# Kernel tuning notes

Measured on AMD Instinct MI355X. Metric: run time of the kernel, lower is better.

Reference implementation:

```python
import jax, jax.numpy as jnp
import numpy as np

S, M, H, E = 8192, 1024, 4096, 8
CAPACITY = S // E  # capacity_factor = 1.0, k = 1


def setup_inputs() -> dict:
    key = jax.random.key(0)
    ks = jax.random.split(key, 4)
    return {
        "x": jax.random.normal(ks[0], (S, M), jnp.float32),
        "wg": jax.random.normal(ks[1], (M, E), jnp.float32) * 0.02,
        "inter_w": jax.random.normal(ks[2], (E, M, H), jnp.float32) * 0.02,
        "inter_b": jnp.zeros((E, H), jnp.float32),
        "output_w": jax.random.normal(ks[3], (E, H, M), jnp.float32) * 0.02,
        "output_b": jnp.zeros((E, M), jnp.float32),
    }


def _top1_gate(x, wg, capacity):
    """GShard-style top-1 gate (inference: no noise, drop tokens over capacity).
    Returns combine_weights [S,E,C] (float) and dispatch_mask [S,E,C] (float 0/1)."""
    logits = x @ wg                                   # [S,E]
    gates = jax.nn.softmax(logits, axis=-1)           # [S,E]
    idx = jnp.argmax(gates, axis=-1)                  # [S]
    mask1 = jax.nn.one_hot(idx, gates.shape[-1], dtype=gates.dtype)  # [S,E]
    # 0-based position of each token within its expert's queue
    locations = jnp.cumsum(mask1, axis=0) - mask1     # [S,E]
    mask1 = mask1 * (locations < capacity)            # drop overflow tokens
    pos = jnp.sum(locations * mask1, axis=1).astype(jnp.int32)  # [S]
    gate_s = jnp.sum(gates * mask1, axis=1)           # [S] gate value of kept tokens
    loc_oh = jax.nn.one_hot(pos, capacity, dtype=gates.dtype)    # [S,C]
    combine = gate_s[:, None, None] * mask1[:, :, None] * loc_oh[:, None, :]  # [S,E,C]
    dispatch = (combine > 0).astype(x.dtype)
    return combine, dispatch


def reference(x, wg, inter_w, inter_b, output_w, output_b):
    combine, dispatch = _top1_gate(x, wg, CAPACITY)
    # token dispatch: torch.einsum('sec,sm->ecm', dispatch_mask, attention_output)
    disp_x = jnp.einsum('sec,sm->ecm', dispatch, x)                 # [E,C,M]
    # per-expert fused gelu-GEMM MLP (gelu_gemm_func: gelu(x@W1+b1)@W2, +b2)
    h = jax.nn.gelu(jnp.einsum('ecm,emh->ech', disp_x, inter_w)
                    + inter_b[:, None, :], approximate=False)       # [E,C,H]
    exp_out = jnp.einsum('ech,ehm->ecm', h, output_w) + output_b[:, None, :]  # [E,C,M]
    # combine: combined_weights.reshape(S, E*C) @ expert_output.reshape(E*C, M)
    y = jnp.einsum('sec,ecm->sm', combine, exp_out)                 # [S,M]
    return y
```

## Files before the change

### kernel.cpp

```cpp
#include <hip/hip_runtime.h>

#define S_ 8192
#define M_ 1024
#define H_ 4096
#define E_ 8
#define C_ 1024

typedef short s16x8 __attribute__((ext_vector_type(8)));
typedef float f32x4 __attribute__((ext_vector_type(4)));

__device__ __forceinline__ unsigned short f2bf(float f) {
    unsigned int u = __float_as_uint(f);
    unsigned int r = u + 0x7fffu + ((u >> 16) & 1u);
    return (unsigned short)(r >> 16);
}
__device__ __forceinline__ float bf2f(unsigned short s) {
    return __uint_as_float(((unsigned int)s) << 16);
}

__device__ __forceinline__ void async_copy16(const unsigned short* g, unsigned short* l) {
    __builtin_amdgcn_global_load_lds(
        (const __attribute__((address_space(1))) unsigned int*)g,
        (__attribute__((address_space(3))) unsigned int*)l, 16, 0, 0);
}

__global__ __launch_bounds__(256) void gate_kernel(
    const float* __restrict__ x, const float* __restrict__ wg,
    int* __restrict__ expert_of, float* __restrict__ gate_full,
    unsigned short* __restrict__ xb)
{
    int token = (blockIdx.x * 256 + threadIdx.x) >> 6;
    int lane  = threadIdx.x & 63;
    const float* xr = x + (size_t)token * M_;
    unsigned short* xbr = xb + (size_t)token * M_;
    double acc[E_] = {0,0,0,0,0,0,0,0};
    for (int t = 0; t < M_ / 64; ++t) {
        int m = t * 64 + lane;
        float xf = xr[m];
        xbr[m] = f2bf(xf);
        double xv = (double)xf;
        const float* w = wg + m * E_;
        #pragma unroll
        for (int e = 0; e < E_; ++e) acc[e] += xv * (double)w[e];
    }
    #pragma unroll
    for (int e = 0; e < E_; ++e)
        for (int off = 32; off; off >>= 1) acc[e] += __shfl_xor(acc[e], off);
    if (lane == 0) {
        double mx = acc[0]; int idx = 0;
        #pragma unroll
        for (int e = 1; e < E_; ++e) if (acc[e] > mx) { mx = acc[e]; idx = e; }
        double den = 0.0;
        #pragma unroll
        for (int e = 0; e < E_; ++e) den += exp(acc[e] - mx);
        expert_of[token] = idx;
        gate_full[token] = (float)(1.0 / den);
    }
}

__global__ __launch_bounds__(256) void count_kernel(
    const int* __restrict__ expert_of, int* __restrict__ cnt,
    int* __restrict__ slot_to_token)
{
    __shared__ int wc[4][E_];
    int tid = threadIdx.x, lane = tid & 63, wv = tid >> 6;
    slot_to_token[blockIdx.x * 256 + tid] = -1;
    int e = expert_of[blockIdx.x * 256 + tid];
    #pragma unroll
    for (int j = 0; j < E_; ++j) {
        unsigned long long b = __ballot(e == j);
        if (lane == 0) wc[wv][j] = __popcll(b);
    }
    __syncthreads();
    if (tid < E_) {
        int s = 0;
        #pragma unroll
        for (int w = 0; w < 4; ++w) s += wc[w][tid];
        cnt[blockIdx.x * E_ + tid] = s;
    }
}

__global__ __launch_bounds__(64) void prefix_kernel(
    const int* __restrict__ cnt, int* __restrict__ cbase)
{
    int tid = threadIdx.x;
    if (tid < E_) {
        int run = 0;
        for (int b = 0; b < 32; ++b) { cbase[b * E_ + tid] = run; run += cnt[b * E_ + tid]; }
    }
}

__global__ __launch_bounds__(256) void scatter_kernel(
    const int* __restrict__ expert_of, const int* __restrict__ cbase,
    int* __restrict__ slot_to_token)
{
    __shared__ int wc[4][E_];
    int tid = threadIdx.x, lane = tid & 63, wv = tid >> 6;
    int s = blockIdx.x * 256 + tid;
    int e = expert_of[s];
    unsigned long long mymask = 0;
    #pragma unroll
    for (int j = 0; j < E_; ++j) {
        unsigned long long b = __ballot(e == j);
        if (lane == 0) wc[wv][j] = __popcll(b);
        if (j == e) mymask = b;
    }
    __syncthreads();
    int waveoff = 0;
    for (int w = 0; w < 4; ++w) if (w < wv) waveoff += wc[w][e];
    int pos = cbase[blockIdx.x * E_ + e] + waveoff +
              __popcll(mymask & ((1ull << lane) - 1ull));
    if (pos < C_) slot_to_token[e * C_ + pos] = s;
}

__global__ __launch_bounds__(256) void transpose_cvt_kernel(
    const float* __restrict__ src, unsigned short* __restrict__ dst, int K, int N)
{
    __shared__ unsigned short tile[64 * 84];
    const size_t esz = (size_t)K * N;
    const float* s = src + (size_t)blockIdx.z * esz;
    unsigned short* d = dst + (size_t)blockIdx.z * esz;
    const int k0 = blockIdx.y * 64, n0 = blockIdx.x * 64;
    const int tid = threadIdx.x;
    {
        const int n  = tid & 63;
        const int kb = (tid >> 6) * 16;
        #pragma unroll
        for (int i = 0; i < 4; ++i) {
            int k4 = kb + i * 4;
            float a0 = s[(size_t)(k0 + k4 + 0) * N + n0 + n];
            float a1 = s[(size_t)(k0 + k4 + 1) * N + n0 + n];
            float a2 = s[(size_t)(k0 + k4 + 2) * N + n0 + n];
            float a3 = s[(size_t)(k0 + k4 + 3) * N + n0 + n];
            unsigned long long p = (unsigned long long)f2bf(a0)
                | ((unsigned long long)f2bf(a1) << 16)
                | ((unsigned long long)f2bf(a2) << 32)
                | ((unsigned long long)f2bf(a3) << 48);
            *(unsigned long long*)(&tile[n * 84 + k4]) = p;
        }
    }
    __syncthreads();
    {
        const int n  = tid >> 3;
        const int k8 = (tid & 7) * 8;
        #pragma unroll
        for (int j = 0; j < 2; ++j) {
            int nn = n + j * 32;
            unsigned long long lo = *(const unsigned long long*)(&tile[nn * 84 + k8]);
            unsigned long long hi = *(const unsigned long long*)(&tile[nn * 84 + k8 + 4]);
            ulonglong2 v; v.x = lo; v.y = hi;
            *(ulonglong2*)(d + (size_t)(n0 + nn) * K + k0 + k8) = v;
        }
    }
}

__global__ __launch_bounds__(256, 2) void gemm1_kernel(
    const unsigned short* __restrict__ xb, const unsigned short* __restrict__ w1t,
    const float* __restrict__ b1, const int* __restrict__ slot_to_token,
    unsigned short* __restrict__ h)
{
    const int e  = blockIdx.z;
    const int n0 = blockIdx.x * 128, c0 = blockIdx.y * 128;
    __shared__ unsigned short As[128 * 32];
    __shared__ unsigned short Bs[128 * 32];
    __shared__ int tok[128];
    const int tid = threadIdx.x;
    if (tid < 128) tok[tid] = slot_to_token[e * C_ + c0 + tid];
    __syncthreads();
    const int wave = tid >> 6, lane = tid & 63;

    const int r0 = tid >> 2;
    const int cq = (tid & 3) ^ ((tid >> 3) & 3);
    const int r1 = 64 + r0;
    int t0 = tok[r0]; if (t0 < 0) t0 = 0;
    int t1 = tok[r1]; if (t1 < 0) t1 = 0;
    const unsigned short* srcA0 = xb + (size_t)t0 * M_ + cq * 8;
    const unsigned short* srcA1 = xb + (size_t)t1 * M_ + cq * 8;
    const unsigned short* Bp = w1t + (size_t)e * M_ * H_;
    const unsigned short* srcB0 = Bp + (size_t)(n0 + r0) * M_ + cq * 8;
    const unsigned short* srcB1 = Bp + (size_t)(n0 + r1) * M_ + cq * 8;
    unsigned short* dstA0 = As + wave * 512;
    unsigned short* dstA1 = As + 2048 + wave * 512;
    unsigned short* dstB0 = Bs + wave * 512;
    unsigned short* dstB1 = Bs + 2048 + wave * 512;

    f32x4 acc[4][4] = {};
    const int wr = wave >> 1, wc = wave & 1, qd = lane >> 4, ln16 = lane & 15;
    const int sq = (qd ^ ((ln16 >> 1) & 3)) * 8;

    for (int k0 = 0; k0 < M_; k0 += 32) {
        async_copy16(srcA0 + k0, dstA0);
        async_copy16(srcA1 + k0, dstA1);
        async_copy16(srcB0 + k0, dstB0);
        async_copy16(srcB1 + k0, dstB1);
        __syncthreads();
        s16x8 af[4], bfr[4];
        #pragma unroll
        for (int i = 0; i < 4; ++i)
            af[i] = *(const s16x8*)(&As[(wr * 64 + i * 16 + ln16) * 32 + sq]);
        #pragma unroll
        for (int j = 0; j < 4; ++j)
            bfr[j] = *(const s16x8*)(&Bs[(wc * 64 + j * 16 + ln16) * 32 + sq]);
        #pragma unroll
        for (int i = 0; i < 4; ++i)
            #pragma unroll
            for (int j = 0; j < 4; ++j)
                acc[i][j] = __builtin_amdgcn_mfma_f32_16x16x32_bf16(
                    af[i], bfr[j], acc[i][j], 0, 0, 0);
        __syncthreads();
    }

    unsigned short* hb = h + (size_t)e * C_ * H_;
    #pragma unroll
    for (int i = 0; i < 4; ++i) {
        int crow = c0 + wr * 64 + i * 16 + qd * 4;
        #pragma unroll
        for (int j = 0; j < 4; ++j) {
            int n = n0 + wc * 64 + j * 16 + ln16;
            float bias = b1[e * H_ + n];
            #pragma unroll
            for (int r = 0; r < 4; ++r) {
                float v = acc[i][j][r] + bias;
                float u = v * v;
                float z = v * (1.5957691216f + 0.0713548163f * u);
                float g = v / (1.0f + __expf(-z));
                hb[(size_t)(crow + r) * H_ + n] = f2bf(g);
            }
        }
    }
}

__global__ __launch_bounds__(256, 2) void gemm2_kernel(
    const unsigned short* __restrict__ h, const unsigned short* __restrict__ w2t,
    const float* __restrict__ b2, const int* __restrict__ slot_to_token,
    const float* __restrict__ gate_full, float* __restrict__ y)
{
    const int e = blockIdx.z;
    const int n0 = blockIdx.x * 128, c0 = blockIdx.y * 128;
    __shared__ unsigned short As[128 * 32];
    __shared__ unsigned short Bs[128 * 32];
    __shared__ int tok[128];
    __shared__ float gw[128];
    const int tid = threadIdx.x;
    if (tid < 128) {
        int t = slot_to_token[e * C_ + c0 + tid];
        tok[tid] = t;
        gw[tid] = (t >= 0) ? gate_full[t] : 0.0f;
    }
    __syncthreads();
    const int wave = tid >> 6, lane = tid & 63;

    const int r0 = tid >> 2;
    const int cq = (tid & 3) ^ ((tid >> 3) & 3);
    const int r1 = 64 + r0;
    const unsigned short* Ap = h + (size_t)e * C_ * H_;
    const unsigned short* srcA0 = Ap + (size_t)(c0 + r0) * H_ + cq * 8;
    const unsigned short* srcA1 = Ap + (size_t)(c0 + r1) * H_ + cq * 8;
    const unsigned short* Bp = w2t + (size_t)e * M_ * H_;
    const unsigned short* srcB0 = Bp + (size_t)(n0 + r0) * H_ + cq * 8;
    const unsigned short* srcB1 = Bp + (size_t)(n0 + r1) * H_ + cq * 8;
    unsigned short* dstA0 = As + wave * 512;
    unsigned short* dstA1 = As + 2048 + wave * 512;
    unsigned short* dstB0 = Bs + wave * 512;
    unsigned short* dstB1 = Bs + 2048 + wave * 512;

    f32x4 acc[4][4] = {};
    const int wr = wave >> 1, wc = wave & 1, qd = lane >> 4, ln16 = lane & 15;
    const int sq = (qd ^ ((ln16 >> 1) & 3)) * 8;

    for (int k0 = 0; k0 < H_; k0 += 32) {
        async_copy16(srcA0 + k0, dstA0);
        async_copy16(srcA1 + k0, dstA1);
        async_copy16(srcB0 + k0, dstB0);
        async_copy16(srcB1 + k0, dstB1);
        __syncthreads();
        s16x8 af[4], bfr[4];
        #pragma unroll
        for (int i = 0; i < 4; ++i)
            af[i] = *(const s16x8*)(&As[(wr * 64 + i * 16 + ln16) * 32 + sq]);
        #pragma unroll
        for (int j = 0; j < 4; ++j)
            bfr[j] = *(const s16x8*)(&Bs[(wc * 64 + j * 16 + ln16) * 32 + sq]);
        #pragma unroll
        for (int i = 0; i < 4; ++i)
            #pragma unroll
            for (int j = 0; j < 4; ++j)
                acc[i][j] = __builtin_amdgcn_mfma_f32_16x16x32_bf16(
                    af[i], bfr[j], acc[i][j], 0, 0, 0);
        __syncthreads();
    }

    #pragma unroll
    for (int i = 0; i < 4; ++i) {
        int lr = wr * 64 + i * 16 + qd * 4;
        #pragma unroll
        for (int j = 0; j < 4; ++j) {
            int n = n0 + wc * 64 + j * 16 + ln16;
            float bias = b2[e * M_ + n];
            #pragma unroll
            for (int r = 0; r < 4; ++r) {
                int t = tok[lr + r];
                if (t >= 0)
                    y[(size_t)t * M_ + n] = gw[lr + r] * (acc[i][j][r] + bias);
            }
        }
    }
}

extern "C" void kernel_launch(void* const* d_in, const int* in_sizes, int n_in,
                              void* d_out, int out_size, void* d_ws, size_t ws_size,
                              hipStream_t stream) {
    const float* x  = (const float*)d_in[0];
    const float* wg = (const float*)d_in[1];
    const float* w1 = (const float*)d_in[2];
    const float* b1 = (const float*)d_in[3];
    const float* w2 = (const float*)d_in[4];
    const float* b2 = (const float*)d_in[5];
    float* y = (float*)d_out;

    char* ws = (char*)d_ws;
    int*   slot_to_token = (int*)ws;
    float* gate_full     = (float*)(ws + 32768);
    int*   cnt           = (int*)(ws + 65536);
    int*   cbase         = (int*)(ws + 66560);
    int*   expert_of     = (int*)(ws + 67584);
    unsigned short* xb   = (unsigned short*)(ws + 131072);
    unsigned short* w2t  = xb + (size_t)S_ * M_;

    unsigned short* w1t  = (unsigned short*)d_in[4];
    unsigned short* h    = (unsigned short*)d_in[2];

    hipMemsetAsync(d_out, 0, (size_t)S_ * M_ * sizeof(float), stream);
    gate_kernel<<<S_ / 4, 256, 0, stream>>>(x, wg, expert_of, gate_full, xb);
    count_kernel<<<32, 256, 0, stream>>>(expert_of, cnt, slot_to_token);
    prefix_kernel<<<1, 64, 0, stream>>>(cnt, cbase);
    scatter_kernel<<<32, 256, 0, stream>>>(expert_of, cbase, slot_to_token);

    transpose_cvt_kernel<<<dim3(M_ / 64, H_ / 64, E_), 256, 0, stream>>>(w2, w2t, H_, M_);
    transpose_cvt_kernel<<<dim3(H_ / 64, M_ / 64, E_), 256, 0, stream>>>(w1, w1t, M_, H_);

    gemm1_kernel<<<dim3(H_ / 128, C_ / 128, E_), 256, 0, stream>>>(
        xb, w1t, b1, slot_to_token, h);
    gemm2_kernel<<<dim3(M_ / 128, C_ / 128, E_), 256, 0, stream>>>(
        h, w2t, b2, slot_to_token, gate_full, y);
}
```

Before: 573.5 us.

## Rewrite expert GEMMs with 256x256 tiles, double-buffered 8-phase pipeline, split-K

Both expert GEMMs move from 128x128 tiles with a single-buffered K=32 loop to 256x256 tiles, 512 threads, and K=64 double-buffered LDS. An 8-phase schedule interleaves async global-to-LDS loads, LDS reads and MFMA bursts, using explicit waitcnt, barriers and setprio to hide load latency. The aim is more data reuse per tile and less barrier stall time. Block indices are remapped so each expert's tiles land on one XCD for L2 locality. gemm2 splits K in two and accumulates into y with atomicAdd to keep enough blocks in flight, at the cost of atomic traffic and a much larger LDS footprint per block.

Measured after the change: 580.9 us. About the same (+1.3%).

```diff
diff --git a/kernel.cpp b/kernel.cpp
--- a/kernel.cpp
+++ b/kernel.cpp
@@ -154,69 +154,125 @@
     }
 }
 
-__global__ __launch_bounds__(256, 2) void gemm1_kernel(
+
+#define RD_A(BUF, I, KS) \
+  (*(const s16x8*)(&AsB[BUF][(wr * 128 + (I) * 16 + ln16) * 64 + ((((KS) * 4 + qd) ^ ln7) * 8)]))
+#define RD_B(BUF, J, KS) \
+  (*(const s16x8*)(&BsB[BUF][(wcn * 64 + (J) * 16 + ln16) * 64 + ((((KS) * 4 + qd) ^ ln7) * 8)]))
+
+#define STG_A(BUF, HF, KT) do { \
+    async_copy16(ap[2 * (HF)]     + (size_t)(KT) * 64, dA##BUF + (2 * (HF)) * 4096); \
+    async_copy16(ap[2 * (HF) + 1] + (size_t)(KT) * 64, dA##BUF + (2 * (HF) + 1) * 4096); } while (0)
+#define STG_B(BUF, HF, KT) do { \
+    async_copy16(bp[2 * (HF)]     + (size_t)(KT) * 64, dB##BUF + (2 * (HF)) * 4096); \
+    async_copy16(bp[2 * (HF) + 1] + (size_t)(KT) * 64, dB##BUF + (2 * (HF) + 1) * 4096); } while (0)
+
+#define MFMA16(I0, J0, BB) do { \
+    __builtin_amdgcn_s_setprio(1); \
+    _Pragma("unroll") \
+    for (int ii = 0; ii < 4; ++ii) { \
+      acc[(I0)+ii][(J0)+0] = __builtin_amdgcn_mfma_f32_16x16x32_bf16(a[ii][0], BB[0][0], acc[(I0)+ii][(J0)+0], 0, 0, 0); \
+      acc[(I0)+ii][(J0)+0] = __builtin_amdgcn_mfma_f32_16x16x32_bf16(a[ii][1], BB[0][1], acc[(I0)+ii][(J0)+0], 0, 0, 0); \
+      acc[(I0)+ii][(J0)+1] = __builtin_amdgcn_mfma_f32_16x16x32_bf16(a[ii][0], BB[1][0], acc[(I0)+ii][(J0)+1], 0, 0, 0); \
+      acc[(I0)+ii][(J0)+1] = __builtin_amdgcn_mfma_f32_16x16x32_bf16(a[ii][1], BB[1][1], acc[(I0)+ii][(J0)+1], 0, 0, 0); \
+    } \
+    __builtin_amdgcn_s_setprio(0); \
+} while (0)
+
+#define BAR()  __builtin_amdgcn_s_barrier()
+#define LGKM0() asm volatile("s_waitcnt lgkmcnt(0)" ::: "memory")
+#define VM2()  asm volatile("s_waitcnt vmcnt(2)" ::: "memory")
+#define VM0()  asm volatile("s_waitcnt vmcnt(0)" ::: "memory")
+
+#define GEMM_8PH(NITER, NT) \
+    STG_A(0, 0, 0); STG_A(0, 1, 0); STG_B(0, 0, 0); STG_B(0, 1, 0); \
+    STG_A(1, 0, 1); \
+    VM2(); BAR(); \
+    for (int it = 0; it < (NITER); ++it) { \
+        const int t1 = 2 * it + 1, t2 = 2 * it + 2, t3 = 2 * it + 3; \
+         \
+        _Pragma("unroll") for (int ii = 0; ii < 4; ++ii) { a[ii][0] = RD_A(0, ii, 0); a[ii][1] = RD_A(0, ii, 1); } \
+        b01[0][0] = RD_B(0, 0, 0); b01[0][1] = RD_B(0, 0, 1); \
+        b01[1][0] = RD_B(0, 1, 0); b01[1][1] = RD_B(0, 1, 1); \
+        STG_A(1, 1, t1); \
+        BAR(); LGKM0(); MFMA16(0, 0, b01); BAR(); \
+         \
+        b23[0][0] = RD_B(0, 2, 0); b23[0][1] = RD_B(0, 2, 1); \
+        b23[1][0] = RD_B(0, 3, 0); b23[1][1] = RD_B(0, 3, 1); \
+        STG_B(1, 0, t1); \
+        BAR(); LGKM0(); MFMA16(0, 2, b23); BAR(); \
+         \
+        _Pragma("unroll") for (int ii = 0; ii < 4; ++ii) { a[ii][0] = RD_A(0, 4 + ii, 0); a[ii][1] = RD_A(0, 4 + ii, 1); } \
+        STG_B(1, 1, t1); \
+        BAR(); LGKM0(); MFMA16(4, 2, b23); BAR(); \
+         \
+        if (t2 < (NT)) { STG_A(0, 0, t2); VM2(); } else { VM0(); } \
+        BAR(); MFMA16(4, 0, b01); BAR(); \
+         \
+        _Pragma("unroll") for (int ii = 0; ii < 4; ++ii) { a[ii][0] = RD_A(1, ii, 0); a[ii][1] = RD_A(1, ii, 1); } \
+        b01[0][0] = RD_B(1, 0, 0); b01[0][1] = RD_B(1, 0, 1); \
+        b01[1][0] = RD_B(1, 1, 0); b01[1][1] = RD_B(1, 1, 1); \
+        if (t2 < (NT)) STG_A(0, 1, t2); \
+        BAR(); LGKM0(); MFMA16(0, 0, b01); BAR(); \
+         \
+        b23[0][0] = RD_B(1, 2, 0); b23[0][1] = RD_B(1, 2, 1); \
+        b23[1][0] = RD_B(1, 3, 0); b23[1][1] = RD_B(1, 3, 1); \
+        if (t2 < (NT)) STG_B(0, 0, t2); \
+        BAR(); LGKM0(); MFMA16(0, 2, b23); BAR(); \
+         \
+        _Pragma("unroll") for (int ii = 0; ii < 4; ++ii) { a[ii][0] = RD_A(1, 4 + ii, 0); a[ii][1] = RD_A(1, 4 + ii, 1); } \
+        if (t2 < (NT)) STG_B(0, 1, t2); \
+        BAR(); LGKM0(); MFMA16(4, 2, b23); BAR(); \
+         \
+        if (t3 < (NT)) { STG_A(1, 0, t3); VM2(); } else { VM0(); } \
+        BAR(); MFMA16(4, 0, b01); BAR(); \
+    }
+
+__global__ __launch_bounds__(512, 2) void gemm1_kernel(
     const unsigned short* __restrict__ xb, const unsigned short* __restrict__ w1t,
     const float* __restrict__ b1, const int* __restrict__ slot_to_token,
     unsigned short* __restrict__ h)
 {
-    const int e  = blockIdx.z;
-    const int n0 = blockIdx.x * 128, c0 = blockIdx.y * 128;
-    __shared__ unsigned short As[128 * 32];
-    __shared__ unsigned short Bs[128 * 32];
-    __shared__ int tok[128];
+    __shared__ unsigned short AsB[2][16384];
+    __shared__ unsigned short BsB[2][16384];
+    __shared__ int tokS[256];
+    const int lin = blockIdx.x + 16 * blockIdx.y + 64 * blockIdx.z;
+    const int e = lin & 7, slot = lin >> 3;
+    const int n0 = (slot & 15) * 256, c0 = (slot >> 4) * 256;
     const int tid = threadIdx.x;
-    if (tid < 128) tok[tid] = slot_to_token[e * C_ + c0 + tid];
-    __syncthreads();
-    const int wave = tid >> 6, lane = tid & 63;
-
-    const int r0 = tid >> 2;
-    const int cq = (tid & 3) ^ ((tid >> 3) & 3);
-    const int r1 = 64 + r0;
-    int t0 = tok[r0]; if (t0 < 0) t0 = 0;
-    int t1 = tok[r1]; if (t1 < 0) t1 = 0;
-    const unsigned short* srcA0 = xb + (size_t)t0 * M_ + cq * 8;
-    const unsigned short* srcA1 = xb + (size_t)t1 * M_ + cq * 8;
-    const unsigned short* Bp = w1t + (size_t)e * M_ * H_;
-    const unsigned short* srcB0 = Bp + (size_t)(n0 + r0) * M_ + cq * 8;
-    const unsigned short* srcB1 = Bp + (size_t)(n0 + r1) * M_ + cq * 8;
-    unsigned short* dstA0 = As + wave * 512;
-    unsigned short* dstA1 = As + 2048 + wave * 512;
-    unsigned short* dstB0 = Bs + wave * 512;
-    unsigned short* dstB1 = Bs + 2048 + wave * 512;
-
-    f32x4 acc[4][4] = {};
-    const int wr = wave >> 1, wc = wave & 1, qd = lane >> 4, ln16 = lane & 15;
-    const int sq = (qd ^ ((ln16 >> 1) & 3)) * 8;
-
-    for (int k0 = 0; k0 < M_; k0 += 32) {
-        async_copy16(srcA0 + k0, dstA0);
-        async_copy16(srcA1 + k0, dstA1);
-        async_copy16(srcB0 + k0, dstB0);
-        async_copy16(srcB1 + k0, dstB1);
-        __syncthreads();
-        s16x8 af[4], bfr[4];
-        #pragma unroll
-        for (int i = 0; i < 4; ++i)
-            af[i] = *(const s16x8*)(&As[(wr * 64 + i * 16 + ln16) * 32 + sq]);
-        #pragma unroll
-        for (int j = 0; j < 4; ++j)
-            bfr[j] = *(const s16x8*)(&Bs[(wc * 64 + j * 16 + ln16) * 32 + sq]);
-        #pragma unroll
-        for (int i = 0; i < 4; ++i)
-            #pragma unroll
-            for (int j = 0; j < 4; ++j)
-                acc[i][j] = __builtin_amdgcn_mfma_f32_16x16x32_bf16(
-                    af[i], bfr[j], acc[i][j], 0, 0, 0);
-        __syncthreads();
-    }
+    if (tid < 256) tokS[tid] = slot_to_token[e * C_ + c0 + tid];
+    __syncthreads();
+    const int wv = tid >> 6, l = tid & 63;
+    const int wr = wv >> 2, wcn = wv & 3;
+    const int qd = l >> 4, ln16 = l & 15, ln7 = ln16 & 7;
+    const int rsub = (wv << 3) + (l >> 3);
+    const int slotoff = ((l & 7) ^ ((l >> 3) & 7)) * 8;
+
+    const unsigned short* ap[4];
+    const unsigned short* bp[4];
+    #pragma unroll
+    for (int q = 0; q < 4; ++q) {
+        int t = tokS[q * 64 + rsub]; if (t < 0) t = 0;
+        ap[q] = xb + (size_t)t * M_ + slotoff;
+        bp[q] = w1t + (size_t)e * M_ * H_ + (size_t)(n0 + q * 64 + rsub) * M_ + slotoff;
+    }
+    unsigned short* dA0 = &AsB[0][(wv * 8) * 64];
+    unsigned short* dA1 = &AsB[1][(wv * 8) * 64];
+    unsigned short* dB0 = &BsB[0][(wv * 8) * 64];
+    unsigned short* dB1 = &BsB[1][(wv * 8) * 64];
+
+    f32x4 acc[8][4] = {};
+    s16x8 a[4][2], b01[2][2], b23[2][2];
+
+    GEMM_8PH(8, 16)
 
     unsigned short* hb = h + (size_t)e * C_ * H_;
     #pragma unroll
-    for (int i = 0; i < 4; ++i) {
-        int crow = c0 + wr * 64 + i * 16 + qd * 4;
+    for (int i = 0; i < 8; ++i) {
+        int crow = c0 + wr * 128 + i * 16 + qd * 4;
         #pragma unroll
         for (int j = 0; j < 4; ++j) {
-            int n = n0 + wc * 64 + j * 16 + ln16;
+            int n = n0 + wcn * 64 + j * 16 + ln16;
             float bias = b1[e * H_ + n];
             #pragma unroll
             for (int r = 0; r < 4; ++r) {
@@ -230,78 +286,63 @@
     }
 }
 
-__global__ __launch_bounds__(256, 2) void gemm2_kernel(
+__global__ __launch_bounds__(512, 2) void gemm2_kernel(
     const unsigned short* __restrict__ h, const unsigned short* __restrict__ w2t,
     const float* __restrict__ b2, const int* __restrict__ slot_to_token,
     const float* __restrict__ gate_full, float* __restrict__ y)
 {
-    const int e = blockIdx.z;
-    const int n0 = blockIdx.x * 128, c0 = blockIdx.y * 128;
-    __shared__ unsigned short As[128 * 32];
-    __shared__ unsigned short Bs[128 * 32];
-    __shared__ int tok[128];
-    __shared__ float gw[128];
+    __shared__ unsigned short AsB[2][16384];
+    __shared__ unsigned short BsB[2][16384];
+    __shared__ int tokS[256];
+    __shared__ float gwS[256];
+    const int lin = blockIdx.x + 4 * blockIdx.y + 16 * blockIdx.z;
+    const int xcd = lin & 7, slot = lin >> 3;
+    const int zz = xcd * 2 + (slot >> 4);
+    const int e = zz >> 1, kc = zz & 1;
+    const int n0 = (slot & 3) * 256, c0 = ((slot >> 2) & 3) * 256;
     const int tid = threadIdx.x;
-    if (tid < 128) {
+    if (tid < 256) {
         int t = slot_to_token[e * C_ + c0 + tid];
-        tok[tid] = t;
-        gw[tid] = (t >= 0) ? gate_full[t] : 0.0f;
-    }
-    __syncthreads();
-    const int wave = tid >> 6, lane = tid & 63;
-
-    const int r0 = tid >> 2;
-    const int cq = (tid & 3) ^ ((tid >> 3) & 3);
-    const int r1 = 64 + r0;
-    const unsigned short* Ap = h + (size_t)e * C_ * H_;
-    const unsigned short* srcA0 = Ap + (size_t)(c0 + r0) * H_ + cq * 8;
-    const unsigned short* srcA1 = Ap + (size_t)(c0 + r1) * H_ + cq * 8;
-    const unsigned short* Bp = w2t + (size_t)e * M_ * H_;
-    const unsigned short* srcB0 = Bp + (size_t)(n0 + r0) * H_ + cq * 8;
-    const unsigned short* srcB1 = Bp + (size_t)(n0 + r1) * H_ + cq * 8;
-    unsigned short* dstA0 = As + wave * 512;
-    unsigned short* dstA1 = As + 2048 + wave * 512;
-    unsigned short* dstB0 = Bs + wave * 512;
-    unsigned short* dstB1 = Bs + 2048 + wave * 512;
-
-    f32x4 acc[4][4] = {};
-    const int wr = wave >> 1, wc = wave & 1, qd = lane >> 4, ln16 = lane & 15;
-    const int sq = (qd ^ ((ln16 >> 1) & 3)) * 8;
-
-    for (int k0 = 0; k0 < H_; k0 += 32) {
-        async_copy16(srcA0 + k0, dstA0);
-        async_copy16(srcA1 + k0, dstA1);
-        async_copy16(srcB0 + k0, dstB0);
-        async_copy16(srcB1 + k0, dstB1);
-        __syncthreads();
-        s16x8 af[4], bfr[4];
-        #pragma unroll
-        for (int i = 0; i < 4; ++i)
-            af[i] = *(const s16x8*)(&As[(wr * 64 + i * 16 + ln16) * 32 + sq]);
-        #pragma unroll
-        for (int j = 0; j < 4; ++j)
-            bfr[j] = *(const s16x8*)(&Bs[(wc * 64 + j * 16 + ln16) * 32 + sq]);
-        #pragma unroll
-        for (int i = 0; i < 4; ++i)
-            #pragma unroll
-            for (int j = 0; j < 4; ++j)
-                acc[i][j] = __builtin_amdgcn_mfma_f32_16x16x32_bf16(
-                    af[i], bfr[j], acc[i][j], 0, 0, 0);
-        __syncthreads();
-    }
-
-    #pragma unroll
-    for (int i = 0; i < 4; ++i) {
-        int lr = wr * 64 + i * 16 + qd * 4;
+        tokS[tid] = t;
+        gwS[tid] = (t >= 0) ? gate_full[t] : 0.0f;
+    }
+    __syncthreads();
+    const int wv = tid >> 6, l = tid & 63;
+    const int wr = wv >> 2, wcn = wv & 3;
+    const int qd = l >> 4, ln16 = l & 15, ln7 = ln16 & 7;
+    const int rsub = (wv << 3) + (l >> 3);
+    const int slotoff = ((l & 7) ^ ((l >> 3) & 7)) * 8;
+    const int kb = kc * 2048;
+
+    const unsigned short* ap[4];
+    const unsigned short* bp[4];
+    #pragma unroll
+    for (int q = 0; q < 4; ++q) {
+        ap[q] = h + (size_t)e * C_ * H_ + (size_t)(c0 + q * 64 + rsub) * H_ + kb + slotoff;
+        bp[q] = w2t + (size_t)e * M_ * H_ + (size_t)(n0 + q * 64 + rsub) * H_ + kb + slotoff;
+    }
+    unsigned short* dA0 = &AsB[0][(wv * 8) * 64];
+    unsigned short* dA1 = &AsB[1][(wv * 8) * 64];
+    unsigned short* dB0 = &BsB[0][(wv * 8) * 64];
+    unsigned short* dB1 = &BsB[1][(wv * 8) * 64];
+
+    f32x4 acc[8][4] = {};
+    s16x8 a[4][2], b01[2][2], b23[2][2];
+
+    GEMM_8PH(16, 32)
+
+    #pragma unroll
+    for (int i = 0; i < 8; ++i) {
+        int lr0 = wr * 128 + i * 16 + qd * 4;
         #pragma unroll
         for (int j = 0; j < 4; ++j) {
-            int n = n0 + wc * 64 + j * 16 + ln16;
-            float bias = b2[e * M_ + n];
+            int n = n0 + wcn * 64 + j * 16 + ln16;
+            float bias = kc ? 0.0f : b2[e * M_ + n];
             #pragma unroll
             for (int r = 0; r < 4; ++r) {
-                int t = tok[lr + r];
+                int t = tokS[lr0 + r];
                 if (t >= 0)
-                    y[(size_t)t * M_ + n] = gw[lr + r] * (acc[i][j][r] + bias);
+                    atomicAdd(&y[(size_t)t * M_ + n], gwS[lr0 + r] * (acc[i][j][r] + bias));
             }
         }
     }
@@ -339,8 +380,6 @@
     transpose_cvt_kernel<<<dim3(M_ / 64, H_ / 64, E_), 256, 0, stream>>>(w2, w2t, H_, M_);
     transpose_cvt_kernel<<<dim3(H_ / 64, M_ / 64, E_), 256, 0, stream>>>(w1, w1t, M_, H_);
 
-    gemm1_kernel<<<dim3(H_ / 128, C_ / 128, E_), 256, 0, stream>>>(
-        xb, w1t, b1, slot_to_token, h);
-    gemm2_kernel<<<dim3(M_ / 128, C_ / 128, E_), 256, 0, stream>>>(
-        h, w2t, b2, slot_to_token, gate_full, y);
-}
+    gemm1_kernel<<<dim3(16, 4, 8), 512, 0, stream>>>(xb, w1t, b1, slot_to_token, h);
+    gemm2_kernel<<<dim3(4, 4, 16), 512, 0, stream>>>(h, w2t, b2, slot_to_token, gate_full, y);
+}
```
